# Kernel optimization log

Hardware: AMD Instinct MI355X
Metric: run time of the kernel (lower is better)

## Reference

```python
import jax, jax.numpy as jnp
import numpy as np

NUM_GROUPS = 32
EPS = 1e-6


def group_norm(x, gamma, beta):
    # x: [b, c, t, h, w]
    b, c, t, h, w = x.shape
    xg = x.reshape(b, NUM_GROUPS, c // NUM_GROUPS, t, h, w)
    mean = xg.mean(axis=(2, 3, 4, 5), keepdims=True)
    var = xg.var(axis=(2, 3, 4, 5), keepdims=True)
    xg = (xg - mean) * jax.lax.rsqrt(var + EPS)
    xn = xg.reshape(b, c, t, h, w)
    return xn * gamma[None, :, None, None, None] + beta[None, :, None, None, None]


def conv1x1(x, w, bias):
    # 1x1x1 Conv3d == per-position channel matmul. x: [b,c,t,h,w], w: [cout,cin]
    y = jnp.einsum('oc,bcthw->bothw', w, x)
    return y + bias[None, :, None, None, None]


def setup_inputs() -> dict:
    key = jax.random.key(0)
    ks = jax.random.split(key, 11)
    c = 512
    b, t, h, w = 1, 16, 32, 32
    s = 1.0 / np.sqrt(c)
    return {
        'x': jax.random.normal(ks[0], (b, c, t, h, w), dtype=jnp.float32),
        'gn_gamma': jnp.ones((c,), jnp.float32),
        'gn_beta': jnp.zeros((c,), jnp.float32),
        'wq': jax.random.normal(ks[1], (c, c), jnp.float32) * s,
        'bq': jnp.zeros((c,), jnp.float32),
        'wk': jax.random.normal(ks[2], (c, c), jnp.float32) * s,
        'bk': jnp.zeros((c,), jnp.float32),
        'wv': jax.random.normal(ks[3], (c, c), jnp.float32) * s,
        'bv': jnp.zeros((c,), jnp.float32),
        'wo': jax.random.normal(ks[4], (c, c), jnp.float32) * s,
        'bo': jnp.zeros((c,), jnp.float32),
    }


def reference(x, gn_gamma, gn_beta, wq, bq, wk, bk, wv, bv, wo, bo):
    b, c, t, h, w = x.shape
    h_ = group_norm(x, gn_gamma, gn_beta)
    q = conv1x1(h_, wq, bq)
    k = conv1x1(h_, wk, bk)
    v = conv1x1(h_, wv, bv)
    # per-frame spatial attention: tokens are the h*w grid, batched over (b t)
    n = h * w
    q = q.transpose(0, 2, 3, 4, 1).reshape(b * t, n, c)   # [(bt), n, c]
    k = k.transpose(0, 2, 3, 4, 1).reshape(b * t, n, c)
    v = v.transpose(0, 2, 3, 4, 1).reshape(b * t, n, c)
    scale = float(int(c) ** (-0.5))
    attn = jax.nn.softmax(jnp.einsum('bic,bjc->bij', q, k) * scale, axis=-1)
    out = jnp.einsum('bij,bjc->bic', attn, v)             # [(bt), n, c]
    out = out.reshape(b, t, h, w, c).transpose(0, 4, 1, 2, 3)
    out = conv1x1(out, wo, bo)
    return x + out
```

## Files before the change

kernel.cpp:

```cpp
#include <hip/hip_runtime.h>
#include <hip/hip_bf16.h>

#define CCH   512
#define NPOS  16384
#define NTOK  1024
#define NFRM  16
#define NGRP  32
#define GSZ   (CCH / NGRP)
#define GELEM (GSZ * NPOS)
#define GN_SPLIT 32

typedef unsigned short u16;
typedef unsigned int   u32;
typedef __attribute__((ext_vector_type(8))) short  short8;
typedef __attribute__((ext_vector_type(4))) float  floatx4;

__device__ __forceinline__ float bf2f(u16 u) {
    return __uint_as_float(((u32)u) << 16);
}
__device__ __forceinline__ u16 f2bf(float f) {
    u32 u = __float_as_uint(f);
    u = (u + 0x7fffu + ((u >> 16) & 1u)) >> 16;
    return (u16)u;
}
__device__ __forceinline__ float ldx(const void* p, size_t i, bool f32m) {
    return f32m ? ((const float*)p)[i] : bf2f(((const u16*)p)[i]);
}
__device__ __forceinline__ void gl2lds16(const u16* g, u16* l) {
    __builtin_amdgcn_global_load_lds(
        (const __attribute__((address_space(1))) u32*)g,
        (__attribute__((address_space(3))) u32*)l, 16, 0, 0);
}

__launch_bounds__(256)
__global__ void detect_dtype(const u32* __restrict__ x32, u32* __restrict__ flag) {
    __shared__ int cnt;
    if (threadIdx.x == 0) cnt = 0;
    __syncthreads();
    int c = 0;
    for (int i = threadIdx.x; i < 4096; i += 256) {
        u32 v = x32[i] & 0xFFFFu;
        u32 e = (v >> 7) & 0xFFu;
        if (e >= 0xC8u) c++;
    }
    atomicAdd(&cnt, c);
    __syncthreads();
    if (threadIdx.x == 0) *flag = (cnt > 64) ? 1u : 0u;
}

__launch_bounds__(256)
__global__ void conv_all(const void* w0, const void* w1, const void* w2, const void* w3,
                         const void* b0, const void* b1, const void* b2, const void* b3,
                         u16* __restrict__ wdst, u16* __restrict__ bdst,
                         float* __restrict__ rl,
                         const u32* __restrict__ flag) {
    int b = blockIdx.x;
    if (b > 1024) {
        rl[(b - 1025) * 256 + threadIdx.x] = 0.0f;
        return;
    }
    bool f32m = *flag != 0u;
    if (b < 1024) {
        int wi = b >> 8;
        const void* src = (wi == 0) ? w0 : (wi == 1) ? w1 : (wi == 2) ? w2 : w3;
        int base = (b & 255) * 1024 + threadIdx.x * 4;
        u16* d = wdst + wi * 262144 + base;
        if (f32m) {
            float4 v = *(const float4*)((const float*)src + base);
            ushort4 o;
            o.x = f2bf(v.x); o.y = f2bf(v.y); o.z = f2bf(v.z); o.w = f2bf(v.w);
            *(ushort4*)d = o;
        } else {
            *(ushort4*)d = *(const ushort4*)((const u16*)src + base);
        }
    } else {
        int t = threadIdx.x;
        int bi = t >> 6;
        int off = (t & 63) * 8;
        const void* src = (bi == 0) ? b0 : (bi == 1) ? b1 : (bi == 2) ? b2 : b3;
        u16* d = bdst + bi * 512 + off;
        if (f32m) {
            float4 v1 = *(const float4*)((const float*)src + off);
            float4 v2 = *(const float4*)((const float*)src + off + 4);
            ushort4 o1, o2;
            o1.x = f2bf(v1.x); o1.y = f2bf(v1.y); o1.z = f2bf(v1.z); o1.w = f2bf(v1.w);
            o2.x = f2bf(v2.x); o2.y = f2bf(v2.y); o2.z = f2bf(v2.z); o2.w = f2bf(v2.w);
            *(ushort4*)d = o1; *(ushort4*)(d + 4) = o2;
        } else {
            *(ushort4*)d = *(const ushort4*)((const u16*)src + off);
            *(ushort4*)(d + 4) = *(const ushort4*)((const u16*)src + off + 4);
        }
    }
}

__launch_bounds__(256)
__global__ void gn_partial(const void* __restrict__ x, float2* __restrict__ partials,
                           const u32* __restrict__ flag) {
    __shared__ float sm[8];
    bool f32m = *flag != 0u;
    const int chunk = GELEM / GN_SPLIT;
    size_t base = (size_t)blockIdx.x * chunk;
    float s = 0.f, ss = 0.f;
    if (f32m) {
        const float4* p = (const float4*)((const float*)x + base);
        for (int i = threadIdx.x; i < chunk / 4; i += 256) {
            float4 u = p[i];
            s  += u.x + u.y + u.z + u.w;
            ss += u.x * u.x + u.y * u.y + u.z * u.z + u.w * u.w;
        }
    } else {
        const ushort4* p = (const ushort4*)((const u16*)x + base);
        for (int i = threadIdx.x; i < chunk / 4; i += 256) {
            ushort4 u = p[i];
            float a = bf2f(u.x), b = bf2f(u.y), c = bf2f(u.z), d = bf2f(u.w);
            s  += a + b + c + d;
            ss += a * a + b * b + c * c + d * d;
        }
    }
    int lane = threadIdx.x & 63, w = threadIdx.x >> 6;
    float t = s;
    #pragma unroll
    for (int o = 32; o > 0; o >>= 1) t += __shfl_down(t, o, 64);
    if (lane == 0) sm[w] = t;
    t = ss;
    #pragma unroll
    for (int o = 32; o > 0; o >>= 1) t += __shfl_down(t, o, 64);
    if (lane == 0) sm[4 + w] = t;
    __syncthreads();
    if (threadIdx.x == 0)
        partials[blockIdx.x] = make_float2(sm[0] + sm[1] + sm[2] + sm[3],
                                           sm[4] + sm[5] + sm[6] + sm[7]);
}

__launch_bounds__(256)
__global__ void gn_apply_t(const void* __restrict__ x, const float2* __restrict__ partials,
                           const void* __restrict__ gamma, const void* __restrict__ beta,
                           u16* __restrict__ xt, const u32* __restrict__ flag) {
    bool f32m = *flag != 0u;
    __shared__ float tile[64][65];
    __shared__ float2 cfs[64];
    int p0 = blockIdx.x * 64, c0 = blockIdx.y * 64;
    if (threadIdx.x < 64) {
        int c = c0 + threadIdx.x, g = c >> 4;
        float sum = 0.f, sq = 0.f;
        #pragma unroll 8
        for (int i = 0; i < GN_SPLIT; ++i) {
            float2 p = partials[g * GN_SPLIT + i];
            sum += p.x; sq += p.y;
        }
        float mean = sum * (1.0f / (float)GELEM);
        float var  = fmaxf(sq * (1.0f / (float)GELEM) - mean * mean, 0.0f);
        float rstd = rsqrtf(var + 1e-6f);
        float gm = ldx(gamma, c, f32m), b = ldx(beta, c, f32m);
        float sc = rstd * gm;
        cfs[threadIdx.x] = make_float2(sc, b - mean * sc);
    }
    __syncthreads();
    int lane = threadIdx.x & 63, rg = threadIdx.x >> 6;
    #pragma unroll 4
    for (int i = 0; i < 16; ++i) {
        int row = rg * 16 + i;
        float2 cf = cfs[row];
        float v = ldx(x, (size_t)(c0 + row) * NPOS + p0 + lane, f32m);
        tile[row][lane] = v * cf.x + cf.y;
    }
    __syncthreads();
    #pragma unroll 4
    for (int i = 0; i < 16; ++i) {
        int prow = rg * 16 + i;
        xt[(size_t)(p0 + prow) * CCH + c0 + lane] = f2bf(tile[lane][prow]);
    }
}

#define EPI_QK    0
#define EPI_V     1
#define EPI_SCEXP 2
#define EPI_PV    3
#define EPI_OUT   4

template<int EPI>
__device__ __forceinline__ void gemm128(
    u16* __restrict__ As, u16* __restrict__ Bs,
    const u16* __restrict__ A, const u16* __restrict__ B,
    void* __restrict__ C, const u16* __restrict__ bias,
    const void* __restrict__ resid, const u32* __restrict__ flag,
    float* __restrict__ rl, int m_blk, int n_blk, int f,
    int lda, int ldb, int ldc, int K, long aFS, long bFS, long cFS)
{
    const int tid = threadIdx.x;
    const u16* Ab = A + (size_t)f * aFS + (size_t)m_blk * 128 * lda;
    const u16* Bb = B + (size_t)f * bFS + (size_t)n_blk * 128 * ldb;

    const int wave = tid >> 6, lane = tid & 63;
    const int srow = wave * 32 + (lane >> 3);
    const int schs = ((lane & 7) ^ ((lane >> 3) & 7)) * 8;

    const int wm = (wave >> 1) * 64, wn = (wave & 1) * 64;
    const int l15 = lane & 15, quad = lane >> 4;

    floatx4 acc[4][4] = {};

    for (int kk = 0; kk < K; kk += 64) {
        __syncthreads();
        #pragma unroll
        for (int o = 0; o < 4; ++o) {
            gl2lds16(Ab + (size_t)(srow + o * 8) * lda + kk + schs, &As[wave * 2048 + o * 512]);
            gl2lds16(Bb + (size_t)(srow + o * 8) * ldb + kk + schs, &Bs[wave * 2048 + o * 512]);
        }
        __syncthreads();
        #pragma unroll
        for (int kh = 0; kh < 2; ++kh) {
            short8 af[4], bf[4];
            #pragma unroll
            for (int mi = 0; mi < 4; ++mi) {
                const int row = wm + mi * 16 + l15;
                af[mi] = *(const short8*)&As[row * 64 + (((kh << 2) | quad) ^ (row & 7)) * 8];
            }
            #pragma unroll
            for (int ni = 0; ni < 4; ++ni) {
                const int row = wn + ni * 16 + l15;
                bf[ni] = *(const short8*)&Bs[row * 64 + (((kh << 2) | quad) ^ (row & 7)) * 8];
            }
            #pragma unroll
            for (int mi = 0; mi < 4; ++mi)
                #pragma unroll
                for (int ni = 0; ni < 4; ++ni)
                    acc[mi][ni] = __builtin_amdgcn_mfma_f32_16x16x32_bf16(
                        af[mi], bf[ni], acc[mi][ni], 0, 0, 0);
        }
    }

    const bool f32m = (EPI == EPI_OUT) ? (*flag != 0u) : false;
    const int m_base = m_blk * 128 + wm;
    const int n_base = n_blk * 128 + wn;
    const float scale = 0.044194173824159216f;

    float inv[4][4];
    if (EPI == EPI_PV) {
        #pragma unroll
        for (int mi = 0; mi < 4; ++mi)
            #pragma unroll
            for (int r = 0; r < 4; ++r)
                inv[mi][r] = 1.0f / rl[f * NTOK + m_base + mi * 16 + quad * 4 + r];
    }
    float rs[4][4];
    if (EPI == EPI_SCEXP) {
        #pragma unroll
        for (int mi = 0; mi < 4; ++mi)
            #pragma unroll
            for (int r = 0; r < 4; ++r) rs[mi][r] = 0.0f;
    }

    #pragma unroll
    for (int mi = 0; mi < 4; ++mi) {
        #pragma unroll
        for (int ni = 0; ni < 4; ++ni) {
            int n = n_base + ni * 16 + l15;
            float bn = (EPI == EPI_QK) ? bf2f(bias[n]) : 0.0f;
            #pragma unroll
            for (int r = 0; r < 4; ++r) {
                int m = m_base + mi * 16 + quad * 4 + r;
                float v = acc[mi][ni][r];
                size_t idx = (size_t)f * cFS + (size_t)m * ldc + n;
                if (EPI == EPI_QK) {
                    ((u16*)C)[idx] = f2bf(v + bn);
                } else if (EPI == EPI_V) {
                    ((u16*)C)[idx] = f2bf(v + bf2f(bias[m]));
                } else if (EPI == EPI_SCEXP) {
                    float ex = __expf(v * scale);
                    rs[mi][r] += ex;
                    ((u16*)C)[idx] = f2bf(ex);
                } else if (EPI == EPI_PV) {
                    ((u16*)C)[idx] = f2bf(v * inv[mi][r]);
                } else {
                    float r2 = v + bf2f(bias[m]) + ldx(resid, idx, f32m);
                    if (f32m) ((float*)C)[idx] = r2;
                    else      ((u16*)C)[idx]   = f2bf(r2);
                }
            }
        }
    }

    if (EPI == EPI_SCEXP) {
        #pragma unroll
        for (int mi = 0; mi < 4; ++mi) {
            #pragma unroll
            for (int r = 0; r < 4; ++r) {
                float s = rs[mi][r];
                s += __shfl_xor(s, 1, 64);
                s += __shfl_xor(s, 2, 64);
                s += __shfl_xor(s, 4, 64);
                s += __shfl_xor(s, 8, 64);
                if (l15 == 0)
                    atomicAdd(&rl[f * NTOK + m_base + mi * 16 + quad * 4 + r], s);
            }
        }
    }
}

template<int EPI, bool MX, bool FSW>
__launch_bounds__(256, 3)
__global__ void mfma_gemm(const u16* __restrict__ A, const u16* __restrict__ B,
                          void* __restrict__ C, const u16* __restrict__ bias,
                          const void* __restrict__ resid, const u32* __restrict__ flag,
                          float* __restrict__ rl,
                          int lda, int ldb, int ldc, int K,
                          long aFS, long bFS, long cFS) {
    __shared__ __align__(16) u16 As[128 * 64];
    __shared__ __align__(16) u16 Bs[128 * 64];
    int bxi, byi, f;
    if (FSW) {
        u32 id = (blockIdx.z * gridDim.y + blockIdx.y) * gridDim.x + blockIdx.x;
        u32 T = gridDim.x * gridDim.y * gridDim.z;
        u32 half = T >> 1;
        f = (int)(id & 7u) + ((id >= half) ? 8 : 0);
        u32 l = (id >= half ? id - half : id) >> 3;
        bxi = (int)(l % gridDim.x);
        byi = (int)(l / gridDim.x);
    } else {
        bxi = blockIdx.x; byi = blockIdx.y; f = blockIdx.z;
    }
    gemm128<EPI>(As, Bs, A, B, C, bias, resid, flag, rl,
                 MX ? bxi : byi, MX ? byi : bxi, f, lda, ldb, ldc, K, aFS, bFS, cFS);
}

__launch_bounds__(256, 3)
__global__ void qkv_gemm(const u16* __restrict__ xnt,
                         const u16* __restrict__ wqk, const u16* __restrict__ bqk,
                         u16* __restrict__ qkt,
                         const u16* __restrict__ wv, const u16* __restrict__ bv,
                         u16* __restrict__ vt,
                         const u32* __restrict__ flag) {
    __shared__ __align__(16) u16 As[128 * 64];
    __shared__ __align__(16) u16 Bs[128 * 64];
    if (blockIdx.y < 8) {
        gemm128<EPI_QK>(As, Bs, xnt, wqk, qkt, bqk, nullptr, flag, nullptr,
                        (int)blockIdx.x, (int)blockIdx.y, 0,
                        CCH, CCH, 1024, CCH, 0, 0, 0);
    } else {
        gemm128<EPI_V>(As, Bs, wv, xnt, vt, bv, nullptr, flag, nullptr,
                       (int)blockIdx.y - 8, (int)blockIdx.x, 0,
                       CCH, CCH, NPOS, CCH, 0, 0, 0);
    }
}

template<int EPI, bool FSW>
__launch_bounds__(512, 4)
__global__ void mfma_gemm256(const u16* __restrict__ A, const u16* __restrict__ B,
                             void* __restrict__ C, const u16* __restrict__ bias,
                             const u32* __restrict__ flag, float* __restrict__ rl,
                             int lda, int ldb, int ldc, int K,
                             long aFS, long bFS, long cFS) {
    __shared__ __align__(16) u16 As[256 * 64];
    __shared__ __align__(16) u16 Bs[128 * 64];
    const int tid = threadIdx.x;

    int bxi, byi, f;
    if (FSW) {
        u32 id = (blockIdx.z * gridDim.y + blockIdx.y) * gridDim.x + blockIdx.x;
        u32 T = gridDim.x * gridDim.y * gridDim.z;
        u32 half = T >> 1;
        f = (int)(id & 7u) + ((id >= half) ? 8 : 0);
        u32 l = (id >= half ? id - half : id) >> 3;
        bxi = (int)(l % gridDim.x);
        byi = (int)(l / gridDim.x);
    } else {
        bxi = blockIdx.x; byi = blockIdx.y; f = blockIdx.z;
    }
    const int m_blk = byi;
    const int n_blk = bxi;

    const u16* Ab = A + (size_t)f * aFS + (size_t)m_blk * 256 * lda;
    const u16* Bb = B + (size_t)f * bFS + (size_t)n_blk * 128 * ldb;

    const int wave = tid >> 6, lane = tid & 63;
    const int srowA = wave * 32 + (lane >> 3);
    const int srowB = wave * 16 + (lane >> 3);
    const int schs  = ((lane & 7) ^ ((lane >> 3) & 7)) * 8;

    const int wm = (wave >> 1) * 64, wn = (wave & 1) * 64;
    const int l15 = lane & 15, quad = lane >> 4;

    floatx4 acc[4][4] = {};

    for (int kk = 0; kk < K; kk += 64) {
        __syncthreads();
        #pragma unroll
        for (int o = 0; o < 4; ++o)
            gl2lds16(Ab + (size_t)(srowA + o * 8) * lda + kk + schs,
                     &As[wave * 2048 + o * 512]);
        #pragma unroll
        for (int o = 0; o < 2; ++o)
            gl2lds16(Bb + (size_t)(srowB + o * 8) * ldb + kk + schs,
                     &Bs[wave * 1024 + o * 512]);
        __syncthreads();
        #pragma unroll
        for (int kh = 0; kh < 2; ++kh) {
            short8 af[4], bf[4];
            #pragma unroll
            for (int mi = 0; mi < 4; ++mi) {
                const int row = wm + mi * 16 + l15;
                af[mi] = *(const short8*)&As[row * 64 + (((kh << 2) | quad) ^ (row & 7)) * 8];
            }
            #pragma unroll
            for (int ni = 0; ni < 4; ++ni) {
                const int row = wn + ni * 16 + l15;
                bf[ni] = *(const short8*)&Bs[row * 64 + (((kh << 2) | quad) ^ (row & 7)) * 8];
            }
            #pragma unroll
            for (int mi = 0; mi < 4; ++mi)
                #pragma unroll
                for (int ni = 0; ni < 4; ++ni)
                    acc[mi][ni] = __builtin_amdgcn_mfma_f32_16x16x32_bf16(
                        af[mi], bf[ni], acc[mi][ni], 0, 0, 0);
        }
    }

    const int m_base = m_blk * 256 + wm;
    const int n_base = n_blk * 128 + wn;
    const float scale = 0.044194173824159216f;

    float rs[4][4];
    #pragma unroll
    for (int mi = 0; mi < 4; ++mi)
        #pragma unroll
        for (int r = 0; r < 4; ++r) rs[mi][r] = 0.0f;

    #pragma unroll
    for (int mi = 0; mi < 4; ++mi) {
        #pragma unroll
        for (int ni = 0; ni < 4; ++ni) {
            int n = n_base + ni * 16 + l15;
            #pragma unroll
            for (int r = 0; r < 4; ++r) {
                int m = m_base + mi * 16 + quad * 4 + r;
                float v = acc[mi][ni][r];
                size_t idx = (size_t)f * cFS + (size_t)m * ldc + n;
                float ex = __expf(v * scale);
                rs[mi][r] += ex;
                ((u16*)C)[idx] = f2bf(ex);
            }
        }
    }

    #pragma unroll
    for (int mi = 0; mi < 4; ++mi) {
        #pragma unroll
        for (int r = 0; r < 4; ++r) {
            float s = rs[mi][r];
            s += __shfl_xor(s, 1, 64);
            s += __shfl_xor(s, 2, 64);
            s += __shfl_xor(s, 4, 64);
            s += __shfl_xor(s, 8, 64);
            if (l15 == 0)
                atomicAdd(&rl[f * NTOK + m_base + mi * 16 + quad * 4 + r], s);
        }
    }
}

extern "C" void kernel_launch(void* const* d_in, const int* in_sizes, int n_in,
                              void* d_out, int out_size, void* d_ws, size_t ws_size,
                              hipStream_t stream) {
    const void* x   = d_in[0];
    const void* gam = d_in[1];
    const void* bet = d_in[2];

    char* ws = (char*)d_ws;
    float2* partials = (float2*)(ws + 4096);
    u32*    flag     = (u32*)(ws + 12352);
    u16* cw[4] = { (u16*)(ws + 16384),              (u16*)(ws + 16384 +  524288ull),
                   (u16*)(ws + 16384 + 1048576ull), (u16*)(ws + 16384 + 1572864ull) };
    u16* cb[4] = { (u16*)(ws + 2113536ull),        (u16*)(ws + 2113536ull + 1024),
                   (u16*)(ws + 2113536ull + 2048), (u16*)(ws + 2113536ull + 3072) };
    float* rl  = (float*)(ws + (3ull << 20));
    u16*  xnt  = (u16*)(ws + (4ull  << 20));
    u16*  qkt  = (u16*)(ws + (20ull << 20));
    u16*  vt   = (u16*)(ws + (52ull << 20));
    u16*  pbuf = (u16*)(ws + (68ull << 20));
    u16*  obuf = xnt;

    detect_dtype<<<1, 256, 0, stream>>>((const u32*)x, flag);
    conv_all<<<1089, 256, 0, stream>>>(d_in[3], d_in[5], d_in[7], d_in[9],
                                       d_in[4], d_in[6], d_in[8], d_in[10],
                                       cw[0], cb[0], rl, flag);
    gn_partial<<<NGRP * GN_SPLIT, 256, 0, stream>>>(x, partials, flag);
    gn_apply_t<<<dim3(NPOS / 64, CCH / 64), 256, 0, stream>>>(
        x, partials, gam, bet, xnt, flag);

    qkv_gemm<<<dim3(128, 12), 256, 0, stream>>>(
        xnt, cw[0], cb[0], qkt, cw[2], cb[2], vt, flag);

    dim3 gsc(NTOK / 128, NTOK / 256, NFRM);
    mfma_gemm256<EPI_SCEXP, true><<<gsc, 512, 0, stream>>>(
        qkt, qkt + 512, pbuf, nullptr, flag, rl, 1024, 1024, NTOK, CCH,
        (long)NTOK * 1024, (long)NTOK * 1024, (long)NTOK * NTOK);

    dim3 gpv(CCH / 128, NTOK / 128, NFRM);
    mfma_gemm<EPI_PV, false, true><<<gpv, 256, 0, stream>>>(
        pbuf, vt, obuf, nullptr, nullptr, flag, rl, NTOK, NPOS, CCH, NTOK,
        (long)NTOK * NTOK, NTOK, (long)NTOK * CCH);

    dim3 go(NPOS / 128, CCH / 128, 1);
    mfma_gemm<EPI_OUT, false, false><<<go, 256, 0, stream>>>(
        cw[3], obuf, d_out, cb[3], x, flag, nullptr, CCH, CCH, NPOS, CCH, 0, 0, 0);
}
```

Baseline: 232.7 us.

## Merge dtype detect, weight convert and GN partials; defer softmax normalization to out-proj

Folds the dtype detection, weight/bias conversion, rowsum zeroing and group-norm partial sums into one prep kernel, with every block recomputing the dtype flag locally. This removes two kernel launches and the serial dependency on a separate flag kernel. It also moves the softmax 1/rowsum scaling out of the PV epilogue and into the output-projection epilogue, where it is applied per column (token). That is valid because the out-projection is linear per token, but PV outputs are now stored unnormalized in bf16. The extra 4096-element detection scan in every prep block adds redundant reads, and the zeroing of rl now runs concurrently with GN blocks, which is harmless.

```diff
diff --git a/kernel.cpp b/kernel.cpp
--- a/kernel.cpp
+++ b/kernel.cpp
@@ -32,8 +32,7 @@
         (__attribute__((address_space(3))) u32*)l, 16, 0, 0);
 }
 
-__launch_bounds__(256)
-__global__ void detect_dtype(const u32* __restrict__ x32, u32* __restrict__ flag) {
+__device__ __forceinline__ bool calc_f32m(const u32* __restrict__ x32) {
     __shared__ int cnt;
     if (threadIdx.x == 0) cnt = 0;
     __syncthreads();
@@ -45,21 +44,24 @@
     }
     atomicAdd(&cnt, c);
     __syncthreads();
-    if (threadIdx.x == 0) *flag = (cnt > 64) ? 1u : 0u;
+    return cnt > 64;
 }
 
 __launch_bounds__(256)
-__global__ void conv_all(const void* w0, const void* w1, const void* w2, const void* w3,
+__global__ void prep_all(const void* __restrict__ x,
+                         const void* w0, const void* w1, const void* w2, const void* w3,
                          const void* b0, const void* b1, const void* b2, const void* b3,
                          u16* __restrict__ wdst, u16* __restrict__ bdst,
-                         float* __restrict__ rl,
-                         const u32* __restrict__ flag) {
+                         float* __restrict__ rl, float2* __restrict__ partials,
+                         u32* __restrict__ flag) {
     int b = blockIdx.x;
-    if (b > 1024) {
+    if (b >= 1025 && b < 1089) {
         rl[(b - 1025) * 256 + threadIdx.x] = 0.0f;
         return;
     }
-    bool f32m = *flag != 0u;
+    bool f32m = calc_f32m((const u32*)x);
+    if (b == 0 && threadIdx.x == 0) *flag = f32m ? 1u : 0u;
+
     if (b < 1024) {
         int wi = b >> 8;
         const void* src = (wi == 0) ? w0 : (wi == 1) ? w1 : (wi == 2) ? w2 : w3;
@@ -73,7 +75,7 @@
         } else {
             *(ushort4*)d = *(const ushort4*)((const u16*)src + base);
         }
-    } else {
+    } else if (b == 1024) {
         int t = threadIdx.x;
         int bi = t >> 6;
         int off = (t & 63) * 8;
@@ -90,46 +92,42 @@
             *(ushort4*)d = *(const ushort4*)((const u16*)src + off);
             *(ushort4*)(d + 4) = *(const ushort4*)((const u16*)src + off + 4);
         }
-    }
-}
-
-__launch_bounds__(256)
-__global__ void gn_partial(const void* __restrict__ x, float2* __restrict__ partials,
-                           const u32* __restrict__ flag) {
-    __shared__ float sm[8];
-    bool f32m = *flag != 0u;
-    const int chunk = GELEM / GN_SPLIT;
-    size_t base = (size_t)blockIdx.x * chunk;
-    float s = 0.f, ss = 0.f;
-    if (f32m) {
-        const float4* p = (const float4*)((const float*)x + base);
-        for (int i = threadIdx.x; i < chunk / 4; i += 256) {
-            float4 u = p[i];
-            s  += u.x + u.y + u.z + u.w;
-            ss += u.x * u.x + u.y * u.y + u.z * u.z + u.w * u.w;
-        }
     } else {
-        const ushort4* p = (const ushort4*)((const u16*)x + base);
-        for (int i = threadIdx.x; i < chunk / 4; i += 256) {
-            ushort4 u = p[i];
-            float a = bf2f(u.x), b = bf2f(u.y), c = bf2f(u.z), d = bf2f(u.w);
-            s  += a + b + c + d;
-            ss += a * a + b * b + c * c + d * d;
-        }
-    }
-    int lane = threadIdx.x & 63, w = threadIdx.x >> 6;
-    float t = s;
-    #pragma unroll
-    for (int o = 32; o > 0; o >>= 1) t += __shfl_down(t, o, 64);
-    if (lane == 0) sm[w] = t;
-    t = ss;
-    #pragma unroll
-    for (int o = 32; o > 0; o >>= 1) t += __shfl_down(t, o, 64);
-    if (lane == 0) sm[4 + w] = t;
-    __syncthreads();
-    if (threadIdx.x == 0)
-        partials[blockIdx.x] = make_float2(sm[0] + sm[1] + sm[2] + sm[3],
-                                           sm[4] + sm[5] + sm[6] + sm[7]);
+        __shared__ float sm[8];
+        int bb = b - 1089;
+        const int chunk = GELEM / GN_SPLIT;
+        size_t base = (size_t)bb * chunk;
+        float s = 0.f, ss = 0.f;
+        if (f32m) {
+            const float4* p = (const float4*)((const float*)x + base);
+            for (int i = threadIdx.x; i < chunk / 4; i += 256) {
+                float4 u = p[i];
+                s  += u.x + u.y + u.z + u.w;
+                ss += u.x * u.x + u.y * u.y + u.z * u.z + u.w * u.w;
+            }
+        } else {
+            const ushort4* p = (const ushort4*)((const u16*)x + base);
+            for (int i = threadIdx.x; i < chunk / 4; i += 256) {
+                ushort4 u = p[i];
+                float a = bf2f(u.x), bq = bf2f(u.y), c = bf2f(u.z), d = bf2f(u.w);
+                s  += a + bq + c + d;
+                ss += a * a + bq * bq + c * c + d * d;
+            }
+        }
+        int lane = threadIdx.x & 63, w = threadIdx.x >> 6;
+        float t = s;
+        #pragma unroll
+        for (int o = 32; o > 0; o >>= 1) t += __shfl_down(t, o, 64);
+        if (lane == 0) sm[w] = t;
+        t = ss;
+        #pragma unroll
+        for (int o = 32; o > 0; o >>= 1) t += __shfl_down(t, o, 64);
+        if (lane == 0) sm[4 + w] = t;
+        __syncthreads();
+        if (threadIdx.x == 0)
+            partials[bb] = make_float2(sm[0] + sm[1] + sm[2] + sm[3],
+                                       sm[4] + sm[5] + sm[6] + sm[7]);
+    }
 }
 
 __launch_bounds__(256)
@@ -235,13 +233,11 @@
     const int n_base = n_blk * 128 + wn;
     const float scale = 0.044194173824159216f;
 
-    float inv[4][4];
-    if (EPI == EPI_PV) {
-        #pragma unroll
-        for (int mi = 0; mi < 4; ++mi)
-            #pragma unroll
-            for (int r = 0; r < 4; ++r)
-                inv[mi][r] = 1.0f / rl[f * NTOK + m_base + mi * 16 + quad * 4 + r];
+    float invn4[4];
+    if (EPI == EPI_OUT) {
+        #pragma unroll
+        for (int ni = 0; ni < 4; ++ni)
+            invn4[ni] = 1.0f / rl[n_base + ni * 16 + l15];
     }
     float rs[4][4];
     if (EPI == EPI_SCEXP) {
@@ -271,9 +267,9 @@
                     rs[mi][r] += ex;
                     ((u16*)C)[idx] = f2bf(ex);
                 } else if (EPI == EPI_PV) {
-                    ((u16*)C)[idx] = f2bf(v * inv[mi][r]);
+                    ((u16*)C)[idx] = f2bf(v);
                 } else {
-                    float r2 = v + bf2f(bias[m]) + ldx(resid, idx, f32m);
+                    float r2 = v * invn4[ni] + bf2f(bias[m]) + ldx(resid, idx, f32m);
                     if (f32m) ((float*)C)[idx] = r2;
                     else      ((u16*)C)[idx]   = f2bf(r2);
                 }
@@ -479,11 +475,10 @@
     u16*  pbuf = (u16*)(ws + (68ull << 20));
     u16*  obuf = xnt;
 
-    detect_dtype<<<1, 256, 0, stream>>>((const u32*)x, flag);
-    conv_all<<<1089, 256, 0, stream>>>(d_in[3], d_in[5], d_in[7], d_in[9],
+    prep_all<<<2113, 256, 0, stream>>>(x,
+                                       d_in[3], d_in[5], d_in[7], d_in[9],
                                        d_in[4], d_in[6], d_in[8], d_in[10],
-                                       cw[0], cb[0], rl, flag);
-    gn_partial<<<NGRP * GN_SPLIT, 256, 0, stream>>>(x, partials, flag);
+                                       cw[0], cb[0], rl, partials, flag);
     gn_apply_t<<<dim3(NPOS / 64, CCH / 64), 256, 0, stream>>>(
         x, partials, gam, bet, xnt, flag);
 
@@ -497,10 +492,10 @@
 
     dim3 gpv(CCH / 128, NTOK / 128, NFRM);
     mfma_gemm<EPI_PV, false, true><<<gpv, 256, 0, stream>>>(
-        pbuf, vt, obuf, nullptr, nullptr, flag, rl, NTOK, NPOS, CCH, NTOK,
+        pbuf, vt, obuf, nullptr, nullptr, flag, nullptr, NTOK, NPOS, CCH, NTOK,
         (long)NTOK * NTOK, NTOK, (long)NTOK * CCH);
 
     dim3 go(NPOS / 128, CCH / 128, 1);
     mfma_gemm<EPI_OUT, false, false><<<go, 256, 0, stream>>>(
-        cw[3], obuf, d_out, cb[3], x, flag, nullptr, CCH, CCH, NPOS, CCH, 0, 0, 0);
-}
+        cw[3], obuf, d_out, cb[3], x, flag, rl, CCH, CCH, NPOS, CCH, 0, 0, 0);
+}
```

After: 222.5 us. 1.05x faster.
